# Kernel tuning notes

Hardware: AMD Instinct MI355X
Metric: run time of the kernel (lower is better)

The kernel has to match this reference:

```python
import jax, jax.numpy as jnp
import numpy as np

B, D, K, NC, F = 2048, 256, 256, 64, 512
EPS = 1e-3           # transport_eps
TAU_MIN = 0.01
TAU_DENOM_MIN = 1e-3


def setup_inputs() -> dict:
    key = jax.random.key(0)
    ks = jax.random.split(key, 8)
    # latents strictly inside the Poincare ball (norm ~0.5 for D=256)
    z = 0.03 * jax.random.normal(ks[0], (B, D), jnp.float32)
    features = jax.random.normal(ks[1], (B, F), jnp.float32)
    # SpectralLinear params (treated as plain linear layers in the reference)
    W_qz = 0.02 * jax.random.normal(ks[2], (K, D), jnp.float32)
    b_qz = jnp.zeros((K,), jnp.float32)
    W_qf = 0.02 * jax.random.normal(ks[3], (K, F), jnp.float32)
    b_qf = jnp.zeros((K,), jnp.float32)
    # full tensorization gamma: [K, D, D]
    q_gamma = 0.02 * jax.random.normal(ks[4], (K, D, D), jnp.float32)
    chart_queries = 0.02 * jax.random.normal(ks[5], (NC, K), jnp.float32)
    return {
        "z": z, "features": features,
        "W_qz": W_qz, "b_qz": b_qz, "W_qf": W_qf, "b_qf": b_qf,
        "q_gamma": q_gamma, "chart_queries": chart_queries,
    }


def reference(z, features, W_qz, b_qz, W_qf, b_qf, q_gamma, chart_queries):
    # centers = chart_queries[:, :latent_dim] (chart_tokens=None path); D == K here
    centers = chart_queries[:, :D]                      # [NC, D]

    # ---- hyperbolic (Poincare ball) distance scores ----
    r2 = jnp.sum(z * z, axis=-1)                        # [B]
    c_sq = jnp.sum(centers * centers, axis=-1)          # [NC]
    diff = z[:, None, :] - centers[None, :, :]          # [B, NC, D]
    dist_sq = jnp.sum(diff * diff, axis=-1)             # [B, NC]
    denom = (1.0 - r2[:, None]) * (1.0 - c_sq[None, :])
    arg = 1.0 + 2.0 * dist_sq / (denom + EPS)
    dist = jnp.arccosh(jnp.maximum(arg, 1.0 + EPS))

    # metric-aware temperature tau(z)
    tau = jnp.maximum(
        jnp.sqrt(jnp.float32(K)) * jnp.maximum(1.0 - r2, TAU_DENOM_MIN) * 0.5,
        TAU_MIN,
    )                                                   # [B]
    scores = -dist / tau[:, None]                       # [B, NC]

    # ---- feature-based refinement (q_feat_proj branch) ----
    q = z @ W_qz.T + b_qz + features @ W_qf.T + b_qf    # [B, K]
    # gamma term: einsum('bij,kij->bk', z outer z, q_gamma) without [B,D,D]
    gz = jnp.einsum('bj,kij->bki', z, q_gamma)          # [B, K, D]
    q = q + jnp.einsum('bki,bi->bk', gz, z)             # [B, K]

    # transported queries: base_queries / lambda(z); (Q/lam) . q == (q @ Q.T)/lam
    r2c = jnp.minimum(r2, 1.0 - EPS)
    lam = 2.0 / (1.0 - r2c + EPS)                       # [B]
    feature_scores = (q @ chart_queries.T) / lam[:, None]  # [B, NC]

    scores = scores + 0.1 * feature_scores / tau[:, None]

    router_weights = jax.nn.softmax(scores, axis=-1)    # [B, NC]
    K_chart = jnp.argmax(router_weights, axis=-1)       # [B]
    return router_weights, K_chart
```

## Files before the change

### kernel.cpp

```cpp
#include <hip/hip_runtime.h>
#include <hip/hip_bf16.h>
#include <hip/hip_fp16.h>


#define B_SZ 2048
#define D_SZ 256
#define K_SZ 256
#define NC_SZ 64
#define F_SZ 512
#define P_SZ 65536

typedef float  floatx4  __attribute__((ext_vector_type(4)));
typedef float  floatx16 __attribute__((ext_vector_type(16)));
typedef _Float16 h8 __attribute__((ext_vector_type(8)));
typedef __fp16  fp16x2 __attribute__((ext_vector_type(2)));
union H8U4 { uint4 u; h8 h; };

#define WS_BEFF  49152
#define WS_CSQ   49216
#define WS_MH    196736
#define WS_WALL  2293888
#define WS_PART  2351232
#define WS_DOT   6938752

__device__ __forceinline__ unsigned pkrtz_u(float a, float b) {
    fp16x2 r = __builtin_amdgcn_cvt_pkrtz(a, b);
    return __builtin_bit_cast(unsigned, r);
}
__device__ __forceinline__ _Float16 h16rtz(float x) {
    fp16x2 r = __builtin_amdgcn_cvt_pkrtz(x, x);
    return (_Float16)r[0];
}
__device__ __forceinline__ unsigned packh2(_Float16 a, _Float16 b) {
    union { _Float16 h[2]; unsigned u; } r; r.h[0] = a; r.h[1] = b; return r.u;
}

__device__ __forceinline__ void gload16(const void* g, void* l) {
    __builtin_amdgcn_global_load_lds(
        (const __attribute__((address_space(1))) unsigned*)g,
        (__attribute__((address_space(3))) unsigned*)l, 16, 0, 0);
}

__global__ __launch_bounds__(256, 4) void mid_kernel(
        const float* __restrict__ gamma, const float* __restrict__ cq,
        const float* __restrict__ Wqz,  const float* __restrict__ bqz,
        const float* __restrict__ Wqf,  const float* __restrict__ bqf,
        float* __restrict__ ws, _Float16* __restrict__ mh) {
    __shared__ float cqL[64*129];
    const int tid = threadIdx.x;
    const int bid = blockIdx.x;

    if (bid < 1024) {
        const int w = tid >> 6, lane = tid & 63;
        const int ln = lane & 31, half = lane >> 5;
        const int mt = w >> 1, ns = w & 1;
        const int p0 = bid * 64;
        const int iseg = p0 >> 8, j0 = p0 & 255;
        const int rot = bid & 15;

        floatx16 acc;
        #pragma unroll
        for (int r = 0; r < 16; ++r) acc[r] = 0.f;

        const int arow = mt*32 + ln;
        const float* __restrict__ cqrow = cq + arow*256;
        const float* __restrict__ gbase =
            gamma + (size_t)(half*8)*P_SZ + p0 + ns*32 + ln;

        #pragma unroll 2
        for (int t = 0; t < 16; ++t) {
            const int kc = (t + rot) & 15;
            float g[8];
            #pragma unroll
            for (int kk = 0; kk < 8; ++kk)
                g[kk] = gbase[(size_t)(kc*16 + kk)*P_SZ];
            const floatx4* cp = (const floatx4*)(cqrow + kc*16 + half*8);
            floatx4 ca = cp[0], cb = cp[1];
            H8U4 a;
            a.u.x = pkrtz_u(ca[0], ca[1]); a.u.y = pkrtz_u(ca[2], ca[3]);
            a.u.z = pkrtz_u(cb[0], cb[1]); a.u.w = pkrtz_u(cb[2], cb[3]);
            H8U4 b;
            b.u.x = pkrtz_u(g[0], g[1]);
            b.u.y = pkrtz_u(g[2], g[3]);
            b.u.z = pkrtz_u(g[4], g[5]);
            b.u.w = pkrtz_u(g[6], g[7]);
            acc = __builtin_amdgcn_mfma_f32_32x32x16_f16(a.h, b.h, acc, 0, 0, 0);
        }
        #pragma unroll
        for (int r = 0; r < 16; ++r) {
            const int cc = mt*32 + (r&3) + 8*(r>>2) + 4*half;
            const int j  = j0 + ns*32 + ln;
            const int jc = j >> 3, off = j & 7;
            mh[(size_t)cc*P_SZ + iseg*256 + ((jc ^ (cc&31))*8 + off)] =
                (_Float16)acc[r];
        }
        return;
    }

    const int pbid = bid - 1024;
    const int w = tid >> 6, c = tid & 63;
    char* wall = (char*)(ws + WS_WALL);

    float a0 = 0.f, a1 = 0.f, a2 = 0.f, a3 = 0.f;
    float bacc = 0.f, cacc = 0.f, cqv = 0.f;
    const int i_or_j = (pbid < 64) ? pbid*4 + w :
                       (pbid < 192) ? (pbid - 64)*4 + w : 0;

    for (int h = 0; h < 2; ++h) {
        #pragma unroll
        for (int s8 = 0; s8 < 8; ++s8) {
            const int e4 = s8*256 + tid;
            const int row = e4 >> 5, col4 = (e4 & 31)*4;
            floatx4 v = *(const floatx4*)(cq + row*256 + h*128 + col4);
            #pragma unroll
            for (int u = 0; u < 4; ++u) cqL[row*129 + col4 + u] = v[u];
        }
        __syncthreads();

        if (pbid < 64) {
            const int i = i_or_j;
            #pragma unroll 8
            for (int kk = 0; kk < 128; kk += 4) {
                const int k = h*128 + kk;
                a0 = fmaf(cqL[c*129 + kk    ], Wqz[(k    )*D_SZ + i], a0);
                a1 = fmaf(cqL[c*129 + kk + 1], Wqz[(k + 1)*D_SZ + i], a1);
                a2 = fmaf(cqL[c*129 + kk + 2], Wqz[(k + 2)*D_SZ + i], a2);
                a3 = fmaf(cqL[c*129 + kk + 3], Wqz[(k + 3)*D_SZ + i], a3);
            }
            if ((i >> 7) == h) cqv = cqL[c*129 + (i & 127)];
        } else if (pbid < 192) {
            const int j = i_or_j;
            #pragma unroll 8
            for (int kk = 0; kk < 128; kk += 4) {
                const int k = h*128 + kk;
                a0 = fmaf(cqL[c*129 + kk    ], Wqf[(k    )*F_SZ + j], a0);
                a1 = fmaf(cqL[c*129 + kk + 1], Wqf[(k + 1)*F_SZ + j], a1);
                a2 = fmaf(cqL[c*129 + kk + 2], Wqf[(k + 2)*F_SZ + j], a2);
                a3 = fmaf(cqL[c*129 + kk + 3], Wqf[(k + 3)*F_SZ + j], a3);
            }
        } else {
            if (w == 0) {
                for (int kk = 0; kk < 128; ++kk) {
                    const int k = h*128 + kk;
                    bacc = fmaf(cqL[c*129 + kk], bqz[k] + bqf[k], bacc);
                }
            } else if (w == 1) {
                for (int ii = 0; ii < 128; ++ii) {
                    const float v = cqL[c*129 + ii];
                    cacc = fmaf(v, v, cacc);
                }
            }
        }
        __syncthreads();
    }

    if (pbid < 64) {
        const int i = i_or_j;
        const int boff = c*512 + ((((i >> 3) & 31) ^ (c & 31)) << 4) + (i & 7)*2;
        *(_Float16*)(wall + 0*32768 + boff) = (_Float16)((a0 + a1) + (a2 + a3));
        const _Float16 vh = (_Float16)cqv;
        *(_Float16*)(wall + 5*32768 + boff) = vh;
        *(_Float16*)(wall + 6*32768 + boff) = h16rtz((cqv - (float)vh) * 1024.f);
    } else if (pbid < 192) {
        const int j = i_or_j;
        const float acc = (a0 + a1) + (a2 + a3);
        const int row = j & 255;
        const int sbase = (j < 256) ? 1 : 3;
        const int boff = c*512 + ((((row >> 3) & 31) ^ (c & 31)) << 4) + (row & 7)*2;
        const _Float16 ah = (_Float16)acc;
        *(_Float16*)(wall + (size_t)sbase*32768 + boff) = ah;
        *(_Float16*)(wall + (size_t)(sbase + 1)*32768 + boff) =
            h16rtz((acc - (float)ah) * 1024.f);
    } else {
        if (w == 0) ws[WS_BEFF + c] = bacc;
        else if (w == 1) ws[WS_CSQ + c] = cacc;
    }
}

__global__ __launch_bounds__(256, 3) void qflin_kernel(
        const float* __restrict__ z, const float* __restrict__ feat,
        const _Float16* __restrict__ mh, const float* __restrict__ wall_f,
        float* __restrict__ part, float* __restrict__ dot) {
    __shared__ __align__(16) char bt[2][16384];
    const int tid = threadIdx.x;
    const int w = tid >> 6, lane = tid & 63;
    const int ln = lane & 31, half = lane >> 5;

    if (blockIdx.x >= 64) {
        const int bid = blockIdx.x - 64;
        const int xcd = bid & 7;
        const int y   = bid >> 3;
        const int ig  = xcd*4 + (y & 3);
        const int b0  = (y >> 2) * 128;
        const int bb  = b0 + w*32 + ln;

        #define STAGE_Q(ii, hs, sel)                                          \
            _Pragma("unroll")                                                 \
            for (int e0 = 0; e0 < 4; ++e0) {                                  \
                const int e = e0*256 + tid;                                   \
                const int cc = e >> 4, up = e & 15;                           \
                const int u = (((hs) ^ ((cc >> 4) & 1)) << 4) | up;           \
                gload16((const char*)mh +                                     \
                        ((size_t)cc*P_SZ + (size_t)(ii)*256)*2 + u*16,        \
                        bt[sel] + e*16);                                      \
            }

        STAGE_Q(ig*8, 0, 0);

        uint4 zjh[16];
        #pragma unroll
        for (int ch = 0; ch < 16; ++ch) {
            const floatx4* zp = (const floatx4*)(z + bb*D_SZ + ch*16 + half*8);
            floatx4 a = zp[0], b = zp[1];
            zjh[ch].x = pkrtz_u(a[0], a[1]);
            zjh[ch].y = pkrtz_u(a[2], a[3]);
            zjh[ch].z = pkrtz_u(b[0], b[1]);
            zjh[ch].w = pkrtz_u(b[2], b[3]);
        }
        float ziv[8];
        {
            const floatx4* zp = (const floatx4*)(z + bb*D_SZ + ig*8);
            floatx4 a = zp[0], b = zp[1];
            #pragma unroll
            for (int t = 0; t < 4; ++t) { ziv[t] = a[t]; ziv[4+t] = b[t]; }
        }

        floatx16 acc0, acc1;
        #pragma unroll
        for (int r = 0; r < 16; ++r) { acc0[r] = 0.f; acc1[r] = 0.f; }

        for (int t = 0; t < 16; ++t) {
            __syncthreads();
            if (t < 15) {
                const int tn = t + 1;
                STAGE_Q(ig*8 + (tn >> 1), tn & 1, tn & 1);
            }
            const int il = t >> 1, hs = t & 1;
            const float zi = ziv[il];
            const unsigned zu = pkrtz_u(zi, zi);
            H8U4 zb; zb.u.x = zu; zb.u.y = zu; zb.u.z = zu; zb.u.w = zu;
            const char* btc = bt[t & 1];
            __builtin_amdgcn_s_setprio(1);
            #pragma unroll
            for (int chp = 0; chp < 8; ++chp) {
                H8U4 aj; aj.u = zjh[hs*8 + chp];
                h8 af = aj.h * zb.h;
                const int po = (((chp*2 + half) ^ (ln & 15)) << 4);
                H8U4 f0, f1;
                f0.u = *(const uint4*)(btc + ln*256 + po);
                f1.u = *(const uint4*)(btc + 8192 + ln*256 + po);
                acc0 = __builtin_amdgcn_mfma_f32_32x32x16_f16(af, f0.h, acc0, 0, 0, 0);
                acc1 = __builtin_amdgcn_mfma_f32_32x32x16_f16(af, f1.h, acc1, 0, 0, 0);
            }
            __builtin_amdgcn_s_setprio(0);
        }
        #undef STAGE_Q

        float* __restrict__ qp = part + (size_t)ig * (B_SZ * NC_SZ);
        #pragma unroll
        for (int r = 0; r < 16; ++r) {
            const int row  = (r&3) + 8*(r>>2) + 4*half;
            const int brow = b0 + w*32 + row;
            qp[brow*NC_SZ + ln]      = acc0[r];
            qp[brow*NC_SZ + 32 + ln] = acc1[r];
        }
        return;
    }

    const char* wall = (const char*)wall_f;
    const int lbid = blockIdx.x;
    const int b0 = (lbid >> 2) * 128;
    const int s  = lbid & 3;
    const int bb = b0 + w*32 + ln;
    const int s_hi = (s == 0) ? 0 : (s == 1) ? 1 : (s == 2) ? 3 : 5;
    const float* __restrict__ arow =
        (s == 0 || s == 3) ? z + bb*D_SZ : feat + bb*F_SZ + (s == 2 ? 256 : 0);

    #define STAGE_L(img, h, sel)                                              \
        _Pragma("unroll")                                                     \
        for (int e0 = 0; e0 < 4; ++e0) {                                      \
            const int e = e0*256 + tid;                                       \
            const int cc = e >> 4, up = e & 15;                               \
            const int u = (((h) ^ ((cc >> 4) & 1)) << 4) | up;                \
            gload16(wall + (size_t)(img)*32768 + cc*512 + u*16,               \
                    bt[sel] + e*16);                                          \
        }

    floatx16 hh0, hh1, lh0, lh1, hl0, hl1;
    #pragma unroll
    for (int r = 0; r < 16; ++r) {
        hh0[r] = 0.f; hh1[r] = 0.f; lh0[r] = 0.f;
        lh1[r] = 0.f; hl0[r] = 0.f; hl1[r] = 0.f;
    }

    for (int h = 0; h < 2; ++h) {
        STAGE_L(s_hi, h, 0);
        if (s > 0) { STAGE_L(s_hi + 1, h, 1); }
        __syncthreads();

        #pragma unroll
        for (int chp = 0; chp < 8; ++chp) {
            const int kb = h*128 + chp*16 + half*8;
            const floatx4* ap = (const floatx4*)(arow + kb);
            floatx4 a4 = ap[0], b4 = ap[1];
            float vv[8];
            #pragma unroll
            for (int t = 0; t < 4; ++t) { vv[t] = a4[t]; vv[4+t] = b4[t]; }
            _Float16 hc[8];
            #pragma unroll
            for (int j = 0; j < 8; ++j) hc[j] = (_Float16)vv[j];
            H8U4 ah;
            ah.u.x = packh2(hc[0], hc[1]); ah.u.y = packh2(hc[2], hc[3]);
            ah.u.z = packh2(hc[4], hc[5]); ah.u.w = packh2(hc[6], hc[7]);

            const int po = (((chp*2 + half) ^ (ln & 15)) << 4);
            H8U4 f0, f1;
            f0.u = *(const uint4*)(bt[0] + ln*256 + po);
            f1.u = *(const uint4*)(bt[0] + 8192 + ln*256 + po);
            hh0 = __builtin_amdgcn_mfma_f32_32x32x16_f16(ah.h, f0.h, hh0, 0, 0, 0);
            hh1 = __builtin_amdgcn_mfma_f32_32x32x16_f16(ah.h, f1.h, hh1, 0, 0, 0);

            if (s > 0) {
                float l[8];
                #pragma unroll
                for (int j = 0; j < 8; ++j) l[j] = (vv[j] - (float)hc[j]) * 1024.f;
                H8U4 al;
                al.u.x = pkrtz_u(l[0], l[1]); al.u.y = pkrtz_u(l[2], l[3]);
                al.u.z = pkrtz_u(l[4], l[5]); al.u.w = pkrtz_u(l[6], l[7]);
                H8U4 g0, g1;
                g0.u = *(const uint4*)(bt[1] + ln*256 + po);
                g1.u = *(const uint4*)(bt[1] + 8192 + ln*256 + po);
                lh0 = __builtin_amdgcn_mfma_f32_32x32x16_f16(al.h, f0.h, lh0, 0, 0, 0);
                lh1 = __builtin_amdgcn_mfma_f32_32x32x16_f16(al.h, f1.h, lh1, 0, 0, 0);
                hl0 = __builtin_amdgcn_mfma_f32_32x32x16_f16(ah.h, g0.h, hl0, 0, 0, 0);
                hl1 = __builtin_amdgcn_mfma_f32_32x32x16_f16(ah.h, g1.h, hl1, 0, 0, 0);
            }
        }
        if (h == 0) __syncthreads();
    }
    #undef STAGE_L

    const float is = 1.0f / 1024.0f;
    float* __restrict__ qp = part + (size_t)(32 + s) * (B_SZ * NC_SZ);
    #pragma unroll
    for (int r = 0; r < 16; ++r) {
        const int row  = (r&3) + 8*(r>>2) + 4*half;
        const int brow = b0 + w*32 + row;
        float v0 = hh0[r], v1 = hh1[r];
        if (s > 0) { v0 += (lh0[r] + hl0[r])*is; v1 += (lh1[r] + hl1[r])*is; }
        if (s < 3) {
            qp[brow*NC_SZ + ln]      = v0;
            qp[brow*NC_SZ + 32 + ln] = v1;
        } else {
            dot[brow*NC_SZ + ln]      = v0;
            dot[brow*NC_SZ + 32 + ln] = v1;
        }
    }
}

__global__ __launch_bounds__(256) void final_kernel(
        const float* __restrict__ z, const float* __restrict__ ws,
        const float* __restrict__ dot, float* __restrict__ out) {
    const int w = threadIdx.x >> 6, c = threadIdx.x & 63;
    const int b = blockIdx.x*4 + w;

    const floatx4 zv = *(const floatx4*)(z + b*D_SZ + c*4);
    float r2 = zv[0]*zv[0] + zv[1]*zv[1] + zv[2]*zv[2] + zv[3]*zv[3];
    #pragma unroll
    for (int off = 32; off > 0; off >>= 1)
        r2 += __shfl_xor(r2, off, 64);

    const float* __restrict__ part = ws + WS_PART;
    float Q = ws[WS_BEFF + c];
    #pragma unroll
    for (int p = 0; p < 35; ++p)
        Q += part[(size_t)p * (B_SZ*NC_SZ) + b*NC_SZ + c];

    const float csq = ws[WS_CSQ + c];
    const float dsq = fmaf(-2.f, dot[b*64 + c], r2) + csq;

    const double r2d = (double)r2, csqd = (double)csq, dsqd = (double)dsq;
    const double denom = (1.0 - r2d) * (1.0 - csqd);
    double arg = 1.0 + 2.0 * dsqd / (denom + 0.001);
    if (arg < 1.001) arg = 1.001;
    const double dist = acosh(arg);
    double tmp = 1.0 - r2d; if (tmp < 0.001) tmp = 0.001;
    double tau = 8.0 * tmp;
    if (tau < 0.01) tau = 0.01;
    double r2c = r2d; if (r2c > 0.999) r2c = 0.999;
    const double lam = 2.0 / (1.0 - r2c + 0.001);
    const double score = -dist / tau + 0.1 * ((double)Q / lam) / tau;

    double m = score;
    #pragma unroll
    for (int off = 32; off > 0; off >>= 1) {
        double o = __shfl_xor(m, off, 64);
        m = fmax(m, o);
    }
    const double e = exp(score - m);
    double s = e;
    #pragma unroll
    for (int off = 32; off > 0; off >>= 1) s += __shfl_xor(s, off, 64);
    out[b*NC_SZ + c] = (float)(e / s);

    double bsc = score; int bix = c;
    #pragma unroll
    for (int off = 32; off > 0; off >>= 1) {
        double osc = __shfl_xor(bsc, off, 64);
        int    oix = __shfl_xor(bix, off, 64);
        if (osc > bsc || (osc == bsc && oix < bix)) { bsc = osc; bix = oix; }
    }
    if (c == 0) out[B_SZ*NC_SZ + b] = (float)bix;
}

extern "C" void kernel_launch(void* const* d_in, const int* in_sizes, int n_in,
                              void* d_out, int out_size, void* d_ws, size_t ws_size,
                              hipStream_t stream) {
    const float* z    = (const float*)d_in[0];
    const float* feat = (const float*)d_in[1];
    const float* Wqz  = (const float*)d_in[2];
    const float* bqz  = (const float*)d_in[3];
    const float* Wqf  = (const float*)d_in[4];
    const float* bqf  = (const float*)d_in[5];
    const float* gamma= (const float*)d_in[6];
    const float* cq   = (const float*)d_in[7];
    float* out = (float*)d_out;
    float* ws  = (float*)d_ws;
    _Float16* mh = (_Float16*)(ws + WS_MH);

    mid_kernel<<<1217, 256, 0, stream>>>(gamma, cq, Wqz, bqz, Wqf, bqf, ws, mh);
    qflin_kernel<<<576, 256, 0, stream>>>(z, feat, mh, ws + WS_WALL,
                                          ws + WS_PART, ws + WS_DOT);
    final_kernel<<<512, 256, 0, stream>>>(z, ws, ws + WS_DOT, out);
}
```

Baseline: 166.0 us.

## Triple-buffer qflin LDS staging with explicit vmcnt waits and nontemporal gamma loads

Replaces the double-buffered LDS staging of the gamma-contracted tensor in the quadratic-term kernel with a three-stage ring. The loop is unrolled, and each step waits with an explicit vmcnt instead of a full __syncthreads drain, so two prefetches stay in flight and global-load latency is better hidden. Separately, gamma reads in the precompute kernel become nontemporal loads to reduce cache pollution from streaming data. The third buffer adds 16KB of LDS per block, which may lower occupancy under launch_bounds(256,3). The hand-tuned vmcnt counts also depend on exact load counts, so they are fragile.

```diff
diff --git a/kernel.cpp b/kernel.cpp
--- a/kernel.cpp
+++ b/kernel.cpp
@@ -73,7 +73,8 @@
             float g[8];
             #pragma unroll
             for (int kk = 0; kk < 8; ++kk)
-                g[kk] = gbase[(size_t)(kc*16 + kk)*P_SZ];
+                g[kk] = __builtin_nontemporal_load(
+                    gbase + (size_t)(kc*16 + kk)*P_SZ);
             const floatx4* cp = (const floatx4*)(cqrow + kc*16 + half*8);
             floatx4 ca = cp[0], cb = cp[1];
             H8U4 a;
@@ -181,7 +182,7 @@
         const float* __restrict__ z, const float* __restrict__ feat,
         const _Float16* __restrict__ mh, const float* __restrict__ wall_f,
         float* __restrict__ part, float* __restrict__ dot) {
-    __shared__ __align__(16) char bt[2][16384];
+    __shared__ __align__(16) char bt[3][16384];
     const int tid = threadIdx.x;
     const int w = tid >> 6, lane = tid & 63;
     const int ln = lane & 31, half = lane >> 5;
@@ -206,6 +207,7 @@
             }
 
         STAGE_Q(ig*8, 0, 0);
+        STAGE_Q(ig*8, 1, 1);
 
         uint4 zjh[16];
         #pragma unroll
@@ -229,31 +231,38 @@
         #pragma unroll
         for (int r = 0; r < 16; ++r) { acc0[r] = 0.f; acc1[r] = 0.f; }
 
-        for (int t = 0; t < 16; ++t) {
-            __syncthreads();
-            if (t < 15) {
-                const int tn = t + 1;
-                STAGE_Q(ig*8 + (tn >> 1), tn & 1, tn & 1);
-            }
-            const int il = t >> 1, hs = t & 1;
-            const float zi = ziv[il];
-            const unsigned zu = pkrtz_u(zi, zi);
-            H8U4 zb; zb.u.x = zu; zb.u.y = zu; zb.u.z = zu; zb.u.w = zu;
-            const char* btc = bt[t & 1];
-            __builtin_amdgcn_s_setprio(1);
-            #pragma unroll
-            for (int chp = 0; chp < 8; ++chp) {
-                H8U4 aj; aj.u = zjh[hs*8 + chp];
-                h8 af = aj.h * zb.h;
-                const int po = (((chp*2 + half) ^ (ln & 15)) << 4);
-                H8U4 f0, f1;
-                f0.u = *(const uint4*)(btc + ln*256 + po);
-                f1.u = *(const uint4*)(btc + 8192 + ln*256 + po);
-                acc0 = __builtin_amdgcn_mfma_f32_32x32x16_f16(af, f0.h, acc0, 0, 0, 0);
-                acc1 = __builtin_amdgcn_mfma_f32_32x32x16_f16(af, f1.h, acc1, 0, 0, 0);
-            }
-            __builtin_amdgcn_s_setprio(0);
-        }
+        #define QF_STEP(T, VMN)                                               \
+        {                                                                     \
+            asm volatile("s_waitcnt vmcnt(" #VMN ")" ::: "memory");           \
+            __builtin_amdgcn_s_barrier();                                     \
+            if ((T) < 14) {                                                   \
+                STAGE_Q(ig*8 + (((T)+2) >> 1), ((T)+2) & 1, ((T)+2) % 3);     \
+            }                                                                 \
+            const int il = (T) >> 1, hs = (T) & 1;                            \
+            const float zi = ziv[il];                                         \
+            const unsigned zu = pkrtz_u(zi, zi);                              \
+            H8U4 zb; zb.u.x = zu; zb.u.y = zu; zb.u.z = zu; zb.u.w = zu;      \
+            const char* btc = bt[(T) % 3];                                    \
+            __builtin_amdgcn_s_setprio(1);                                    \
+            _Pragma("unroll")                                                 \
+            for (int chp = 0; chp < 8; ++chp) {                               \
+                H8U4 aj; aj.u = zjh[hs*8 + chp];                              \
+                h8 af = aj.h * zb.h;                                          \
+                const int po = (((chp*2 + half) ^ (ln & 15)) << 4);           \
+                H8U4 f0, f1;                                                  \
+                f0.u = *(const uint4*)(btc + ln*256 + po);                    \
+                f1.u = *(const uint4*)(btc + 8192 + ln*256 + po);             \
+                acc0 = __builtin_amdgcn_mfma_f32_32x32x16_f16(af, f0.h, acc0, 0, 0, 0); \
+                acc1 = __builtin_amdgcn_mfma_f32_32x32x16_f16(af, f1.h, acc1, 0, 0, 0); \
+            }                                                                 \
+            __builtin_amdgcn_s_setprio(0);                                    \
+        }
+
+        QF_STEP(0, 4);  QF_STEP(1, 4);  QF_STEP(2, 4);  QF_STEP(3, 4);
+        QF_STEP(4, 4);  QF_STEP(5, 4);  QF_STEP(6, 4);  QF_STEP(7, 4);
+        QF_STEP(8, 4);  QF_STEP(9, 4);  QF_STEP(10, 4); QF_STEP(11, 4);
+        QF_STEP(12, 4); QF_STEP(13, 4); QF_STEP(14, 4); QF_STEP(15, 0);
+        #undef QF_STEP
         #undef STAGE_Q
 
         float* __restrict__ qp = part + (size_t)ig * (B_SZ * NC_SZ);
```

After: 196.8 us. +18.5%, slower.

## Stage gamma through LDS with double-buffered async loads and widen per-block tile

Applied to the files above, without the earlier changes.

The gamma-contraction blocks now each cover 128 output columns instead of 64, halving the block count and running two MFMA accumulators per wave that share the A operand. Gamma tiles are brought into shared memory with global_load_lds 16-byte async copies, double-buffered so the next k-chunk loads while the current one computes. Before, each lane issued strided scalar global loads. The change adds a __syncthreads per iteration and more LDS traffic, and removes the per-block k-rotation used to spread memory access.

```diff
diff --git a/kernel.cpp b/kernel.cpp
--- a/kernel.cpp
+++ b/kernel.cpp
@@ -46,58 +46,76 @@
         const float* __restrict__ Wqz,  const float* __restrict__ bqz,
         const float* __restrict__ Wqf,  const float* __restrict__ bqf,
         float* __restrict__ ws, _Float16* __restrict__ mh) {
-    __shared__ float cqL[64*129];
+    __shared__ __align__(16) float cqL[64*129];
     const int tid = threadIdx.x;
     const int bid = blockIdx.x;
 
-    if (bid < 1024) {
+    if (bid < 512) {
         const int w = tid >> 6, lane = tid & 63;
         const int ln = lane & 31, half = lane >> 5;
         const int mt = w >> 1, ns = w & 1;
-        const int p0 = bid * 64;
+        const int p0 = bid * 128;
         const int iseg = p0 >> 8, j0 = p0 & 255;
-        const int rot = bid & 15;
-
-        floatx16 acc;
-        #pragma unroll
-        for (int r = 0; r < 16; ++r) acc[r] = 0.f;
-
-        const int arow = mt*32 + ln;
-        const float* __restrict__ cqrow = cq + arow*256;
-        const float* __restrict__ gbase =
-            gamma + (size_t)(half*8)*P_SZ + p0 + ns*32 + ln;
-
-        #pragma unroll 2
+        char* bt = (char*)cqL;
+
+        floatx16 acc0, acc1;
+        #pragma unroll
+        for (int r = 0; r < 16; ++r) { acc0[r] = 0.f; acc1[r] = 0.f; }
+
+        const float* __restrict__ cqrow = cq + (mt*32 + ln)*256;
+
+        #define STAGE_G(kc, sel)                                              \
+            _Pragma("unroll")                                                 \
+            for (int e0 = 0; e0 < 2; ++e0) {                                  \
+                const int e = e0*256 + tid;                                   \
+                gload16(gamma + (size_t)((kc)*16 + (e >> 5))*P_SZ             \
+                              + p0 + (e & 31)*4,                              \
+                        bt + (sel)*8192 + e*16);                              \
+            }
+
+        STAGE_G(0, 0);
         for (int t = 0; t < 16; ++t) {
-            const int kc = (t + rot) & 15;
-            float g[8];
-            #pragma unroll
-            for (int kk = 0; kk < 8; ++kk)
-                g[kk] = gbase[(size_t)(kc*16 + kk)*P_SZ];
-            const floatx4* cp = (const floatx4*)(cqrow + kc*16 + half*8);
-            floatx4 ca = cp[0], cb = cp[1];
+            __syncthreads();
+            if (t < 15) { STAGE_G(t + 1, (t + 1) & 1); }
+
+            const floatx4* ap = (const floatx4*)(cqrow + t*16 + half*8);
+            floatx4 ca = ap[0], cb = ap[1];
             H8U4 a;
             a.u.x = pkrtz_u(ca[0], ca[1]); a.u.y = pkrtz_u(ca[2], ca[3]);
             a.u.z = pkrtz_u(cb[0], cb[1]); a.u.w = pkrtz_u(cb[2], cb[3]);
-            H8U4 b;
-            b.u.x = pkrtz_u(g[0], g[1]);
-            b.u.y = pkrtz_u(g[2], g[3]);
-            b.u.z = pkrtz_u(g[4], g[5]);
-            b.u.w = pkrtz_u(g[6], g[7]);
-            acc = __builtin_amdgcn_mfma_f32_32x32x16_f16(a.h, b.h, acc, 0, 0, 0);
-        }
+
+            const char* btc = bt + (t & 1)*8192;
+            float g0[8], g1[8];
+            #pragma unroll
+            for (int kk = 0; kk < 8; ++kk) {
+                const int roff = (half*8 + kk)*512;
+                g0[kk] = *(const float*)(btc + roff + (ns*64 + ln)*4);
+                g1[kk] = *(const float*)(btc + roff + (ns*64 + 32 + ln)*4);
+            }
+            H8U4 b0, b1;
+            b0.u.x = pkrtz_u(g0[0], g0[1]); b0.u.y = pkrtz_u(g0[2], g0[3]);
+            b0.u.z = pkrtz_u(g0[4], g0[5]); b0.u.w = pkrtz_u(g0[6], g0[7]);
+            b1.u.x = pkrtz_u(g1[0], g1[1]); b1.u.y = pkrtz_u(g1[2], g1[3]);
+            b1.u.z = pkrtz_u(g1[4], g1[5]); b1.u.w = pkrtz_u(g1[6], g1[7]);
+
+            acc0 = __builtin_amdgcn_mfma_f32_32x32x16_f16(a.h, b0.h, acc0, 0, 0, 0);
+            acc1 = __builtin_amdgcn_mfma_f32_32x32x16_f16(a.h, b1.h, acc1, 0, 0, 0);
+        }
+        #undef STAGE_G
+
         #pragma unroll
         for (int r = 0; r < 16; ++r) {
             const int cc = mt*32 + (r&3) + 8*(r>>2) + 4*half;
-            const int j  = j0 + ns*32 + ln;
-            const int jc = j >> 3, off = j & 7;
-            mh[(size_t)cc*P_SZ + iseg*256 + ((jc ^ (cc&31))*8 + off)] =
-                (_Float16)acc[r];
+            const int ja = j0 + ns*64 + ln;
+            const int jb = j0 + ns*64 + 32 + ln;
+            const size_t base = (size_t)cc*P_SZ + iseg*256;
+            mh[base + (((ja >> 3) ^ (cc&31))*8 + (ja & 7))] = (_Float16)acc0[r];
+            mh[base + (((jb >> 3) ^ (cc&31))*8 + (jb & 7))] = (_Float16)acc1[r];
         }
         return;
     }
 
-    const int pbid = bid - 1024;
+    const int pbid = bid - 512;
     const int w = tid >> 6, c = tid & 63;
     char* wall = (char*)(ws + WS_WALL);
 
@@ -428,7 +446,7 @@
     float* ws  = (float*)d_ws;
     _Float16* mh = (_Float16*)(ws + WS_MH);
 
-    mid_kernel<<<1217, 256, 0, stream>>>(gamma, cq, Wqz, bqz, Wqf, bqf, ws, mh);
+    mid_kernel<<<705, 256, 0, stream>>>(gamma, cq, Wqz, bqz, Wqf, bqf, ws, mh);
     qflin_kernel<<<576, 256, 0, stream>>>(z, feat, mh, ws + WS_WALL,
                                           ws + WS_PART, ws + WS_DOT);
     final_kernel<<<512, 256, 0, stream>>>(z, ws, ws + WS_DOT, out);
```

Result: faster. 152.3 us, median of 2 (-8.2%).
